# Optimization experiments

Measured on AMD Instinct MI355X. Metric: run time of the kernel, lower is better.

Reference implementation:

```python
import jax, jax.numpy as jnp
import numpy as np
import math

RCR = 5.2
RCA = 3.5
NUM_SPECIES = 4
NUM_PAIRS = NUM_SPECIES * (NUM_SPECIES + 1) // 2  # 10
BOX = 10.0  # Angstrom box side


def _triu_index(n):
    s1, s2 = np.triu_indices(n)
    t = np.zeros((n, n), dtype=np.int32)
    idx = np.arange(len(s1))
    t[s1, s2] = idx
    t[s2, s1] = idx
    return jnp.asarray(t)

TRIU = _triu_index(NUM_SPECIES)


def _cutoff_cosine(d, rc):
    return 0.5 * jnp.cos(d * (math.pi / rc)) + 0.5


def _aev(coordinates, EtaR, ShfR, EtaA, Zeta, ShfA, ShfZ, species):
    C, A, _ = coordinates.shape
    # pairwise displacement vec[c,i,j] = r_j - r_i   (c,i,j,3)
    vec = coordinates[:, None, :, :] - coordinates[:, :, None, :]
    d2 = jnp.sum(vec * vec, axis=-1)
    pair_ok = ~jnp.eye(A, dtype=bool)[None]            # exclude self pairs
    d = jnp.sqrt(jnp.where(pair_ok, d2, 1.0))          # safe sqrt for grads

    # ---- radial AEV (eq. 3) ----
    mask_r = pair_ok & (d <= RCR)
    fc = _cutoff_cosine(d, RCR)
    diff = d[..., None] - ShfR                          # (c,i,j,R)
    rad = 0.25 * jnp.exp(-EtaR[0] * diff * diff) * fc[..., None]
    rad = jnp.where(mask_r[..., None], rad, 0.0)
    oh = jax.nn.one_hot(species, NUM_SPECIES, dtype=rad.dtype)  # (c,j,s)
    radial_aev = jnp.einsum('cjs,cijr->cisr', oh, rad).reshape(C, A, -1)

    # ---- angular AEV (eq. 4): center i, neighbor pair (j,k), j<k ----
    mask_nb = pair_ok & (d <= RCA)                      # (c,i,j)
    jk_lt = jnp.triu(jnp.ones((A, A), dtype=bool), 1)   # j < k
    mask_t = mask_nb[:, :, :, None] & mask_nb[:, :, None, :] & jk_lt[None, None]
    d_ij = d[:, :, :, None]
    d_ik = d[:, :, None, :]
    dot = jnp.einsum('cijx,cikx->cijk', vec, vec)
    cos_ang = dot / jnp.maximum(d_ij * d_ik, 1e-10)
    angles = jnp.arccos(0.95 * cos_ang)                 # (c,i,j,k)
    fcj = _cutoff_cosine(d, RCA)
    fcj12 = fcj[:, :, :, None] * fcj[:, :, None, :]
    # factor1: (c,i,j,k,1,SZ) ; factor2: (c,i,j,k,SA,1)
    f1 = ((1.0 + jnp.cos(angles[..., None, None] - ShfZ)) / 2.0) ** Zeta[0]
    e = (d_ij + d_ik) / 2.0
    e = e[..., None] - ShfA                             # (c,i,j,k,SA)
    f2 = jnp.exp(-EtaA[0] * e * e)
    ang = 2.0 * f1 * f2[..., None] * fcj12[..., None, None]
    ang = jnp.where(mask_t[..., None, None], ang, 0.0)
    ang = ang.reshape(C, A, A, A, -1)                   # (c,i,j,k,SA*SZ)
    pidx = TRIU[species[:, :, None], species[:, None, :]]  # (c,j,k)
    ohp = jax.nn.one_hot(pidx, NUM_PAIRS, dtype=ang.dtype)
    angular_aev = jnp.einsum('cjkp,cijkf->cipf', ohp, ang).reshape(C, A, -1)

    return jnp.concatenate([radial_aev, angular_aev], axis=-1)  # (c,a,384)


def setup_inputs() -> dict:
    key = jax.random.key(0)
    k1, k2 = jax.random.split(key)
    C, A = 32, 48
    coordinates = jax.random.uniform(k1, (C, A, 3), dtype=jnp.float32) * BOX
    species = jax.random.randint(k2, (C, A), 0, NUM_SPECIES)
    EtaR = jnp.array([16.0], dtype=jnp.float32)
    ShfR = jnp.linspace(0.9, 5.2, 17, dtype=jnp.float32)[:-1]       # 16 shifts
    EtaA = jnp.array([8.0], dtype=jnp.float32)
    Zeta = jnp.array([32.0], dtype=jnp.float32)
    ShfA = jnp.linspace(0.9, 3.5, 5, dtype=jnp.float32)[:-1]        # 4 shifts
    ShfZ = ((jnp.arange(8, dtype=jnp.float32) + 0.5) * (math.pi / 8.0))  # 8 sections
    return {"coordinates": coordinates, "EtaR": EtaR, "ShfR": ShfR,
            "EtaA": EtaA, "Zeta": Zeta, "ShfA": ShfA, "ShfZ": ShfZ,
            "species": species}


def reference(coordinates, EtaR, ShfR, EtaA, Zeta, ShfA, ShfZ, species):
    aevs = _aev(coordinates, EtaR, ShfR, EtaA, Zeta, ShfA, ShfZ, species)
    return aevs
```

## Files before the change

kernel.cpp:

```cpp
#include <hip/hip_runtime.h>
#include <hip/hip_bf16.h>
#include <math.h>

#define NC 32
#define NA 48
#define NSP 4
#define NPAIRS 10
#define NSHFR 16
#define NSHFA 4
#define NSHFZ 8
#define RAD_LEN (NSP * NSHFR)
#define ANG_LEN (NPAIRS * NSHFA * NSHFZ)
#define AEV_LEN (RAD_LEN + ANG_LEN)

#define RCR 5.2f
#define RCA 3.5f

__global__ __launch_bounds__(64)
void aev_kernel(const float* __restrict__ coords,
                const float* __restrict__ etaR_p,
                const float* __restrict__ shfR,
                const float* __restrict__ etaA_p,
                const float* __restrict__ zeta_p,
                const float* __restrict__ shfA,
                const float* __restrict__ shfZ,
                const int*   __restrict__ species,
                float* __restrict__ out)
{
    const int tid = threadIdx.x;
    const int blk = blockIdx.x;
    const int c = blk / NA;
    const int i = blk - c * NA;

    __shared__ float sx[NA], sy[NA], sz[NA];
    __shared__ int   ssp[NA];
    __shared__ float sd[NA];
    __shared__ int   nb[NA];
    __shared__ float nbd[NA];
    __shared__ int   nM;
    __shared__ float aev[AEV_LEN];
    __shared__ float sCz[NSHFZ], sSz[NSHFZ];
    __shared__ float sShfA[NSHFA];

    for (int f = tid; f < AEV_LEN; f += 64) aev[f] = 0.0f;
    if (tid == 0) nM = 0;
    if (tid < NA) {
        const int g = (c * NA + tid) * 3;
        sx[tid] = coords[g + 0];
        sy[tid] = coords[g + 1];
        sz[tid] = coords[g + 2];
        ssp[tid] = species[c * NA + tid];
    }
    if (tid < NSHFZ) {
        float v = shfZ[tid];
        sCz[tid] = cosf(v);
        sSz[tid] = sinf(v);
    }
    if (tid >= 8 && tid < 8 + NSHFA) sShfA[tid - 8] = shfA[tid - 8];
    __syncthreads();

    const float xi = sx[i], yi = sy[i], zi = sz[i];
    const float etaR = etaR_p[0];
    const float etaA = etaA_p[0];
    const float zeta = zeta_p[0];

    if (tid < NA) {
        float dx = sx[tid] - xi, dy = sy[tid] - yi, dz = sz[tid] - zi;
        float d = sqrtf(dx * dx + dy * dy + dz * dz);
        if (tid == i) d = 1.0e9f;
        sd[tid] = d;
        if (tid != i && d <= RCA) {
            int slot = atomicAdd(&nM, 1);
            nb[slot]  = tid;
            nbd[slot] = d;
        }
    }
    __syncthreads();

    {
        const int s = tid >> 4;
        const int r = tid & 15;
        const float shfr = shfR[r];
        float acc = 0.0f;
        for (int j = 0; j < NA; ++j) {
            float d = sd[j];
            if (d <= RCR && ssp[j] == s) {
                float fc = 0.5f * cosf(d * (float)(M_PI / 5.2)) + 0.5f;
                float diff = d - shfr;
                acc += 0.25f * expf(-etaR * diff * diff) * fc;
            }
        }
        aev[tid] = acc;
    }

    const int M = nM;
    const int npairs = (M * (M - 1)) >> 1;
    for (int p = tid; p < npairs; p += 64) {
        int a = 0, rem = p, rowlen = M - 1;
        while (rem >= rowlen) { rem -= rowlen; --rowlen; ++a; }
        int b = a + 1 + rem;

        const int j = nb[a], k = nb[b];
        const float d1 = nbd[a], d2 = nbd[b];
        float v1x = sx[j] - xi, v1y = sy[j] - yi, v1z = sz[j] - zi;
        float v2x = sx[k] - xi, v2y = sy[k] - yi, v2z = sz[k] - zi;
        float dot = v1x * v2x + v1y * v2y + v1z * v2z;
        float cosang = dot / fmaxf(d1 * d2, 1e-10f);
        cosang = fminf(1.0f, fmaxf(-1.0f, cosang));
        float ct = 0.95f * cosang;
        float st = sqrtf(fmaxf(0.0f, 1.0f - ct * ct));
        float fc1 = 0.5f * cosf(d1 * (float)(M_PI / 3.5)) + 0.5f;
        float fc2 = 0.5f * cosf(d2 * (float)(M_PI / 3.5)) + 0.5f;
        float fcj12 = fc1 * fc2;
        float ebase = 0.5f * (d1 + d2);

        int s1 = ssp[j], s2 = ssp[k];
        int lo = min(s1, s2), hi = max(s1, s2);
        int pidx = lo * NSP - ((lo * (lo - 1)) >> 1) + (hi - lo);

        float f2v[NSHFA];
        #pragma unroll
        for (int a2 = 0; a2 < NSHFA; ++a2) {
            float e = ebase - sShfA[a2];
            f2v[a2] = expf(-etaA * e * e);
        }
        float* basep = &aev[RAD_LEN + pidx * (NSHFA * NSHFZ)];
        #pragma unroll
        for (int z = 0; z < NSHFZ; ++z) {
            float cz = ct * sCz[z] + st * sSz[z];
            float f1 = powf(0.5f * (1.0f + cz), zeta);
            float t = 2.0f * f1 * fcj12;
            #pragma unroll
            for (int a2 = 0; a2 < NSHFA; ++a2) {
                atomicAdd(&basep[a2 * NSHFZ + z], t * f2v[a2]);
            }
        }
    }
    __syncthreads();

    float* o = out + (size_t)blk * AEV_LEN;
    for (int f = tid; f < AEV_LEN; f += 64) {
        o[f] = aev[f];
    }
}

extern "C" void kernel_launch(void* const* d_in, const int* in_sizes, int n_in,
                              void* d_out, int out_size, void* d_ws, size_t ws_size,
                              hipStream_t stream) {
    const float* coords = (const float*)d_in[0];
    const float* etaR   = (const float*)d_in[1];
    const float* shfR   = (const float*)d_in[2];
    const float* etaA   = (const float*)d_in[3];
    const float* zeta   = (const float*)d_in[4];
    const float* shfA   = (const float*)d_in[5];
    const float* shfZ   = (const float*)d_in[6];
    const int*   spec   = (const int*)d_in[7];
    float* out = (float*)d_out;

    aev_kernel<<<NC * NA, 64, 0, stream>>>(coords, etaR, shfR, etaA, zeta,
                                           shfA, shfZ, spec, out);
}
```

Before: 87.82 us.

## Compact radial/angular neighbor lists and split angular work per (pair, zeta-shift)

Builds compacted radial and angular neighbor lists in shared memory with precomputed cutoff values and displacement vectors. Radial terms are computed only over in-cutoff neighbors using fast exp and atomic adds. Angular work becomes two phases per chunk of 64 pairs: per-pair geometry goes into shared memory, then each (pair, ShfZ) task is spread across threads. When zeta is 32 the power is computed by repeated squaring. Output is stored as float4. This adds barriers and more shared-memory atomics, and the fast intrinsics change accuracy slightly.

```diff
diff --git a/kernel.cpp b/kernel.cpp
--- a/kernel.cpp
+++ b/kernel.cpp
@@ -34,16 +34,20 @@
 
     __shared__ float sx[NA], sy[NA], sz[NA];
     __shared__ int   ssp[NA];
-    __shared__ float sd[NA];
-    __shared__ int   nb[NA];
-    __shared__ float nbd[NA];
+    __shared__ float rd[NA], rfc[NA];
+    __shared__ int   rsp[NA];
+    __shared__ int   nR;
+    __shared__ float ax[NA], ay[NA], az[NA], ad[NA], afc[NA];
+    __shared__ int   asp[NA];
     __shared__ int   nM;
-    __shared__ float aev[AEV_LEN];
-    __shared__ float sCz[NSHFZ], sSz[NSHFZ];
-    __shared__ float sShfA[NSHFA];
+    __shared__ float pct[64], pst[64], pfc[64];
+    __shared__ float pf2[NSHFA][64];
+    __shared__ int   ppidx[64];
+    __shared__ float sCz[NSHFZ], sSz[NSHFZ], sShfA[NSHFA], sShfR[NSHFR];
+    alignas(16) __shared__ float aev[AEV_LEN];
 
     for (int f = tid; f < AEV_LEN; f += 64) aev[f] = 0.0f;
-    if (tid == 0) nM = 0;
+    if (tid == 0) { nR = 0; nM = 0; }
     if (tid < NA) {
         const int g = (c * NA + tid) * 3;
         sx[tid] = coords[g + 0];
@@ -56,91 +60,101 @@
         sCz[tid] = cosf(v);
         sSz[tid] = sinf(v);
     }
-    if (tid >= 8 && tid < 8 + NSHFA) sShfA[tid - 8] = shfA[tid - 8];
+    if (tid >= 8 && tid < 8 + NSHFA)  sShfA[tid - 8]  = shfA[tid - 8];
+    if (tid >= 16 && tid < 16 + NSHFR) sShfR[tid - 16] = shfR[tid - 16];
     __syncthreads();
 
     const float xi = sx[i], yi = sy[i], zi = sz[i];
     const float etaR = etaR_p[0];
     const float etaA = etaA_p[0];
     const float zeta = zeta_p[0];
+    const bool  zeta32 = (zeta == 32.0f);
 
-    if (tid < NA) {
+    if (tid < NA && tid != i) {
         float dx = sx[tid] - xi, dy = sy[tid] - yi, dz = sz[tid] - zi;
         float d = sqrtf(dx * dx + dy * dy + dz * dz);
-        if (tid == i) d = 1.0e9f;
-        sd[tid] = d;
-        if (tid != i && d <= RCA) {
+        if (d <= RCR) {
+            float fcR = 0.5f * cosf(d * (float)(M_PI / 5.2)) + 0.5f;
+            int slot = atomicAdd(&nR, 1);
+            rd[slot] = d; rfc[slot] = fcR; rsp[slot] = ssp[tid];
+        }
+        if (d <= RCA) {
+            float fcA = 0.5f * cosf(d * (float)(M_PI / 3.5)) + 0.5f;
             int slot = atomicAdd(&nM, 1);
-            nb[slot]  = tid;
-            nbd[slot] = d;
+            ax[slot] = dx; ay[slot] = dy; az[slot] = dz;
+            ad[slot] = d; afc[slot] = fcA; asp[slot] = ssp[tid];
         }
     }
     __syncthreads();
 
     {
-        const int s = tid >> 4;
-        const int r = tid & 15;
-        const float shfr = shfR[r];
-        float acc = 0.0f;
-        for (int j = 0; j < NA; ++j) {
-            float d = sd[j];
-            if (d <= RCR && ssp[j] == s) {
-                float fc = 0.5f * cosf(d * (float)(M_PI / 5.2)) + 0.5f;
-                float diff = d - shfr;
-                acc += 0.25f * expf(-etaR * diff * diff) * fc;
-            }
+        const int ntask = nR * NSHFR;
+        for (int t = tid; t < ntask; t += 64) {
+            int j = t >> 4, r = t & 15;
+            float diff = rd[j] - sShfR[r];
+            float v = 0.25f * __expf(-etaR * diff * diff) * rfc[j];
+            atomicAdd(&aev[rsp[j] * NSHFR + r], v);
         }
-        aev[tid] = acc;
     }
 
     const int M = nM;
     const int npairs = (M * (M - 1)) >> 1;
-    for (int p = tid; p < npairs; p += 64) {
-        int a = 0, rem = p, rowlen = M - 1;
-        while (rem >= rowlen) { rem -= rowlen; --rowlen; ++a; }
-        int b = a + 1 + rem;
+    for (int p0 = 0; p0 < npairs; p0 += 64) {
+        const int chunk = min(64, npairs - p0);
+        if (tid < chunk) {
+            int p = p0 + tid;
+            int a = 0, rem = p, rowlen = M - 1;
+            while (rem >= rowlen) { rem -= rowlen; --rowlen; ++a; }
+            int b = a + 1 + rem;
 
-        const int j = nb[a], k = nb[b];
-        const float d1 = nbd[a], d2 = nbd[b];
-        float v1x = sx[j] - xi, v1y = sy[j] - yi, v1z = sz[j] - zi;
-        float v2x = sx[k] - xi, v2y = sy[k] - yi, v2z = sz[k] - zi;
-        float dot = v1x * v2x + v1y * v2y + v1z * v2z;
-        float cosang = dot / fmaxf(d1 * d2, 1e-10f);
-        cosang = fminf(1.0f, fmaxf(-1.0f, cosang));
-        float ct = 0.95f * cosang;
-        float st = sqrtf(fmaxf(0.0f, 1.0f - ct * ct));
-        float fc1 = 0.5f * cosf(d1 * (float)(M_PI / 3.5)) + 0.5f;
-        float fc2 = 0.5f * cosf(d2 * (float)(M_PI / 3.5)) + 0.5f;
-        float fcj12 = fc1 * fc2;
-        float ebase = 0.5f * (d1 + d2);
-
-        int s1 = ssp[j], s2 = ssp[k];
-        int lo = min(s1, s2), hi = max(s1, s2);
-        int pidx = lo * NSP - ((lo * (lo - 1)) >> 1) + (hi - lo);
-
-        float f2v[NSHFA];
-        #pragma unroll
-        for (int a2 = 0; a2 < NSHFA; ++a2) {
-            float e = ebase - sShfA[a2];
-            f2v[a2] = expf(-etaA * e * e);
-        }
-        float* basep = &aev[RAD_LEN + pidx * (NSHFA * NSHFZ)];
-        #pragma unroll
-        for (int z = 0; z < NSHFZ; ++z) {
-            float cz = ct * sCz[z] + st * sSz[z];
-            float f1 = powf(0.5f * (1.0f + cz), zeta);
-            float t = 2.0f * f1 * fcj12;
+            float d1 = ad[a], d2 = ad[b];
+            float dot = ax[a] * ax[b] + ay[a] * ay[b] + az[a] * az[b];
+            float cosang = dot / fmaxf(d1 * d2, 1e-10f);
+            cosang = fminf(1.0f, fmaxf(-1.0f, cosang));
+            float ct = 0.95f * cosang;
+            pct[tid] = ct;
+            pst[tid] = sqrtf(fmaxf(0.0f, 1.0f - ct * ct));
+            pfc[tid] = afc[a] * afc[b];
+            int s1 = asp[a], s2 = asp[b];
+            int lo = min(s1, s2), hi = max(s1, s2);
+            ppidx[tid] = lo * NSP - ((lo * (lo - 1)) >> 1) + (hi - lo);
+            float ebase = 0.5f * (d1 + d2);
             #pragma unroll
             for (int a2 = 0; a2 < NSHFA; ++a2) {
-                atomicAdd(&basep[a2 * NSHFZ + z], t * f2v[a2]);
+                float e = ebase - sShfA[a2];
+                pf2[a2][tid] = __expf(-etaA * e * e);
             }
         }
+        __syncthreads();
+
+        const int ntask = chunk * NSHFZ;
+        for (int t = tid; t < ntask; t += 64) {
+            int p = t >> 3, z = t & 7;
+            float ct = pct[p], st = pst[p];
+            float cz = ct * sCz[z] + st * sSz[z];
+            float u = 0.5f * (1.0f + cz);
+            float f1;
+            if (zeta32) {
+                float u2 = u * u, u4 = u2 * u2, u8 = u4 * u4, u16 = u8 * u8;
+                f1 = u16 * u16;
+            } else {
+                f1 = __powf(u, zeta);
+            }
+            float tmul = 2.0f * f1 * pfc[p];
+            float* basep = &aev[RAD_LEN + ppidx[p] * (NSHFA * NSHFZ) + z];
+            #pragma unroll
+            for (int a2 = 0; a2 < NSHFA; ++a2) {
+                atomicAdd(&basep[a2 * NSHFZ], tmul * pf2[a2][p]);
+            }
+        }
+        __syncthreads();
     }
     __syncthreads();
 
-    float* o = out + (size_t)blk * AEV_LEN;
-    for (int f = tid; f < AEV_LEN; f += 64) {
-        o[f] = aev[f];
+    float4* o4 = (float4*)(out + (size_t)blk * AEV_LEN);
+    const float4* a4 = (const float4*)aev;
+    for (int f = tid; f < AEV_LEN / 4; f += 64) {
+        o4[f] = a4[f];
     }
 }
 
```

Measured after the change: 82.52 us. 6.0% less time.
